# Kernel optimization log

Measured on AMD Instinct MI355X. Metric: run time of the kernel, lower is better.

## Reference

```python
import jax, jax.numpy as jnp
import numpy as np

B, N, K = 16, 4096, 128

def setup_inputs() -> dict:
    key = jax.random.key(0)
    k1, k2, k3, k4, k5 = jax.random.split(key, 5)
    positions = jax.random.normal(k1, (B, N, 3), dtype=jnp.float32) * 5.0
    neighbors = jax.random.randint(k2, (B, N, K), 0, N, dtype=jnp.int32)
    neighbor_mask = (jax.random.uniform(k3, (B, N, K)) < 0.9).astype(jnp.float32)
    cell = jax.random.normal(k4, (B, 3, 3), dtype=jnp.float32) + 10.0 * jnp.eye(3, dtype=jnp.float32)
    cell_offsets = jax.random.randint(k5, (B, N, K, 3), -1, 2).astype(jnp.float32)
    return {
        "positions": positions,
        "neighbors": neighbors,
        "neighbor_mask": neighbor_mask,
        "cell": cell,
        "cell_offsets": cell_offsets,
    }

def reference(positions, neighbors, neighbor_mask, cell, cell_offsets):
    # Gather neighbor positions: [B,N,K,3]
    pos_j = jax.vmap(lambda p, n: p[n])(positions, neighbors)
    # Relative vectors r_j - r_i
    dist_vec = pos_j - positions[:, :, None, :]
    # Periodic boundary correction: offsets @ cell, [B,N,K,3]
    dist_vec = dist_vec + jnp.einsum("bnkd,bde->bnke", cell_offsets, cell)
    sq = jnp.sum(dist_vec * dist_vec, axis=-1)  # [B,N,K]
    mask = neighbor_mask > 0
    # Masked distances (safe sqrt: avoid sqrt(0) grad issues on masked entries)
    distances = jnp.where(mask, jnp.sqrt(jnp.where(mask, sq, 1.0)), 0.0)
    return distances
```

## Files before the change

kernel.cpp:

```cpp
#include <hip/hip_runtime.h>
#include <math.h>

constexpr int B = 16;
constexpr int N = 4096;
constexpr int K = 128;

constexpr int ROWS_PER_BLOCK = 256;
constexpr int THREADS = 1024;
constexpr int CHUNKS  = 8;
constexpr int WINDOW  = 4;

typedef float fx4 __attribute__((ext_vector_type(4)));
typedef int   ix4 __attribute__((ext_vector_type(4)));


struct Chunk {
    ix4 jj;
    fx4 mm, o0, o1, o2;
};

__device__ __forceinline__ void load_chunk(Chunk& c,
                                           const int*   __restrict__ nbr,
                                           const float* __restrict__ mask,
                                           const float* __restrict__ offs,
                                           size_t e0) {
    c.jj = __builtin_nontemporal_load((const ix4*)(nbr  + e0));
    c.mm = __builtin_nontemporal_load((const fx4*)(mask + e0));
    c.o0 = __builtin_nontemporal_load((const fx4*)(offs + e0 * 3));
    c.o1 = __builtin_nontemporal_load((const fx4*)(offs + e0 * 3 + 4));
    c.o2 = __builtin_nontemporal_load((const fx4*)(offs + e0 * 3 + 8));
}

__global__ __launch_bounds__(THREADS, 4)
void pairwise_dist_mlp(const float* __restrict__ pos,
                       const int*   __restrict__ nbr,
                       const float* __restrict__ mask,
                       const float* __restrict__ cell,
                       const float* __restrict__ offs,
                       float*       __restrict__ out) {
    __shared__ fx4 spos[N];

    const int tid   = threadIdx.x;
    const int b     = blockIdx.x >> 4;
    const int rblk  = blockIdx.x & 15;
    const int nbase = rblk * ROWS_PER_BLOCK;

    {
        const fx4* __restrict__ pb4 = (const fx4*)(pos + (size_t)b * N * 3);
        const fx4 r0 = pb4[tid * 3 + 0];
        const fx4 r1 = pb4[tid * 3 + 1];
        const fx4 r2 = pb4[tid * 3 + 2];
        const int a0 = tid * 4;
        spos[a0 + 0] = (fx4){r0.x, r0.y, r0.z, 0.f};
        spos[a0 + 1] = (fx4){r0.w, r1.x, r1.y, 0.f};
        spos[a0 + 2] = (fx4){r1.z, r1.w, r2.x, 0.f};
        spos[a0 + 3] = (fx4){r2.y, r2.z, r2.w, 0.f};
    }

    const float* __restrict__ cb = cell + b * 9;
    const float c00 = cb[0], c01 = cb[1], c02 = cb[2];
    const float c10 = cb[3], c11 = cb[4], c12 = cb[5];
    const float c20 = cb[6], c21 = cb[7], c22 = cb[8];

    __syncthreads();

    const size_t blockElemBase = ((size_t)b * N + nbase) * K;

    Chunk win[WINDOW];
#pragma unroll
    for (int c = 0; c < WINDOW; ++c)
        load_chunk(win[c], nbr, mask, offs,
                   blockElemBase + (size_t)c * 4096 + (size_t)tid * 4);

#pragma unroll
    for (int c = 0; c < CHUNKS; ++c) {
        const Chunk cur = win[c % WINDOW];

        const int    eLocal = c * 4096 + tid * 4;
        const size_t e0     = blockElemBase + eLocal;
        const int    n      = nbase + (eLocal >> 7);
        const fx4    pi     = spos[n];

        if (c + WINDOW < CHUNKS)
            load_chunk(win[c % WINDOW], nbr, mask, offs,
                       blockElemBase + (size_t)(c + WINDOW) * 4096 +
                       (size_t)tid * 4);

        const float ox[4] = {cur.o0.x, cur.o0.w, cur.o1.z, cur.o2.y};
        const float oy[4] = {cur.o0.y, cur.o1.x, cur.o1.w, cur.o2.z};
        const float oz[4] = {cur.o0.z, cur.o1.y, cur.o2.x, cur.o2.w};
        const int   j [4] = {cur.jj.x, cur.jj.y, cur.jj.z, cur.jj.w};
        const float m [4] = {cur.mm.x, cur.mm.y, cur.mm.z, cur.mm.w};

        float res[4];
#pragma unroll
        for (int i = 0; i < 4; ++i) {
            const fx4 pj = spos[j[i]];
            const float dx = (pj.x - pi.x) + ox[i] * c00 + oy[i] * c10 + oz[i] * c20;
            const float dy = (pj.y - pi.y) + ox[i] * c01 + oy[i] * c11 + oz[i] * c21;
            const float dz = (pj.z - pi.z) + ox[i] * c02 + oy[i] * c12 + oz[i] * c22;
            const float sq = dx * dx + dy * dy + dz * dz;
            res[i] = (m[i] > 0.0f) ? sqrtf(sq) : 0.0f;
        }

        const fx4 r = {res[0], res[1], res[2], res[3]};
        __builtin_nontemporal_store(r, (fx4*)(out + e0));
    }
}

extern "C" void kernel_launch(void* const* d_in, const int* in_sizes, int n_in,
                              void* d_out, int out_size, void* d_ws, size_t ws_size,
                              hipStream_t stream) {
    const float* positions     = (const float*)d_in[0];
    const int*   neighbors     = (const int*)  d_in[1];
    const float* neighbor_mask = (const float*)d_in[2];
    const float* cell          = (const float*)d_in[3];
    const float* cell_offsets  = (const float*)d_in[4];
    float*       out           = (float*)d_out;

    const int blocks = B * (N / ROWS_PER_BLOCK);

    pairwise_dist_mlp<<<blocks, THREADS, 0, stream>>>(
        positions, neighbors, neighbor_mask, cell, cell_offsets, out);
}
```

Before: 204.1 us.

## Halve block size and issue all chunk loads before the shared-memory barrier

Halves the block to 512 threads over 128 rows and doubles the grid. Every thread now issues all eight chunks of neighbor, mask and offset loads up front, before the barrier that waits for the position table to fill shared memory. This lets global loads overlap the shared-memory fill and the barrier, replacing the rolling four-deep window. The cost is more registers per thread, and the 64KB position table is now rebuilt twice as many times per batch.

```diff
diff --git a/kernel.cpp b/kernel.cpp
--- a/kernel.cpp
+++ b/kernel.cpp
@@ -5,10 +5,9 @@
 constexpr int N = 4096;
 constexpr int K = 128;
 
-constexpr int ROWS_PER_BLOCK = 256;
-constexpr int THREADS = 1024;
+constexpr int ROWS_PER_BLOCK = 128;
+constexpr int THREADS = 512;
 constexpr int CHUNKS  = 8;
-constexpr int WINDOW  = 4;
 
 typedef float fx4 __attribute__((ext_vector_type(4)));
 typedef int   ix4 __attribute__((ext_vector_type(4)));
@@ -31,30 +30,38 @@
     c.o2 = __builtin_nontemporal_load((const fx4*)(offs + e0 * 3 + 8));
 }
 
-__global__ __launch_bounds__(THREADS, 4)
-void pairwise_dist_mlp(const float* __restrict__ pos,
-                       const int*   __restrict__ nbr,
-                       const float* __restrict__ mask,
-                       const float* __restrict__ cell,
-                       const float* __restrict__ offs,
-                       float*       __restrict__ out) {
+__global__ __launch_bounds__(THREADS, 2)
+void pairwise_dist_win8(const float* __restrict__ pos,
+                        const int*   __restrict__ nbr,
+                        const float* __restrict__ mask,
+                        const float* __restrict__ cell,
+                        const float* __restrict__ offs,
+                        float*       __restrict__ out) {
     __shared__ fx4 spos[N];
 
     const int tid   = threadIdx.x;
-    const int b     = blockIdx.x >> 4;
-    const int rblk  = blockIdx.x & 15;
+    const int b     = blockIdx.x >> 5;
+    const int rblk  = blockIdx.x & 31;
     const int nbase = rblk * ROWS_PER_BLOCK;
 
     {
         const fx4* __restrict__ pb4 = (const fx4*)(pos + (size_t)b * N * 3);
-        const fx4 r0 = pb4[tid * 3 + 0];
-        const fx4 r1 = pb4[tid * 3 + 1];
-        const fx4 r2 = pb4[tid * 3 + 2];
-        const int a0 = tid * 4;
+        const int base = tid * 6;
+        const fx4 r0 = pb4[base + 0];
+        const fx4 r1 = pb4[base + 1];
+        const fx4 r2 = pb4[base + 2];
+        const fx4 r3 = pb4[base + 3];
+        const fx4 r4 = pb4[base + 4];
+        const fx4 r5 = pb4[base + 5];
+        const int a0 = tid * 8;
         spos[a0 + 0] = (fx4){r0.x, r0.y, r0.z, 0.f};
         spos[a0 + 1] = (fx4){r0.w, r1.x, r1.y, 0.f};
         spos[a0 + 2] = (fx4){r1.z, r1.w, r2.x, 0.f};
         spos[a0 + 3] = (fx4){r2.y, r2.z, r2.w, 0.f};
+        spos[a0 + 4] = (fx4){r3.x, r3.y, r3.z, 0.f};
+        spos[a0 + 5] = (fx4){r3.w, r4.x, r4.y, 0.f};
+        spos[a0 + 6] = (fx4){r4.z, r4.w, r5.x, 0.f};
+        spos[a0 + 7] = (fx4){r5.y, r5.z, r5.w, 0.f};
     }
 
     const float* __restrict__ cb = cell + b * 9;
@@ -62,29 +69,25 @@
     const float c10 = cb[3], c11 = cb[4], c12 = cb[5];
     const float c20 = cb[6], c21 = cb[7], c22 = cb[8];
 
-    __syncthreads();
-
     const size_t blockElemBase = ((size_t)b * N + nbase) * K;
 
-    Chunk win[WINDOW];
+    Chunk win[CHUNKS];
 #pragma unroll
-    for (int c = 0; c < WINDOW; ++c)
+    for (int c = 0; c < CHUNKS; ++c)
         load_chunk(win[c], nbr, mask, offs,
-                   blockElemBase + (size_t)c * 4096 + (size_t)tid * 4);
+                   blockElemBase + (size_t)c * (THREADS * 4) +
+                   (size_t)tid * 4);
+
+    __syncthreads();
 
 #pragma unroll
     for (int c = 0; c < CHUNKS; ++c) {
-        const Chunk cur = win[c % WINDOW];
+        const Chunk& cur = win[c];
 
-        const int    eLocal = c * 4096 + tid * 4;
+        const int    eLocal = c * (THREADS * 4) + tid * 4;
         const size_t e0     = blockElemBase + eLocal;
         const int    n      = nbase + (eLocal >> 7);
         const fx4    pi     = spos[n];
-
-        if (c + WINDOW < CHUNKS)
-            load_chunk(win[c % WINDOW], nbr, mask, offs,
-                       blockElemBase + (size_t)(c + WINDOW) * 4096 +
-                       (size_t)tid * 4);
 
         const float ox[4] = {cur.o0.x, cur.o0.w, cur.o1.z, cur.o2.y};
         const float oy[4] = {cur.o0.y, cur.o1.x, cur.o1.w, cur.o2.z};
@@ -120,6 +123,6 @@
 
     const int blocks = B * (N / ROWS_PER_BLOCK);
 
-    pairwise_dist_mlp<<<blocks, THREADS, 0, stream>>>(
+    pairwise_dist_win8<<<blocks, THREADS, 0, stream>>>(
         positions, neighbors, neighbor_mask, cell, cell_offsets, out);
 }
```

Result: no change. 207.7 us (+1.8%).
